# Kernel tuning notes

Measured on AMD Instinct MI355X. Metric: run time of the kernel, lower is better.

## Reference

```python
import jax, jax.numpy as jnp
import numpy as np

B, LQ, LK = 4, 2048, 2048
DQ = DK = DV = DH = 1024


def _xavier(key, shape):
    fan_out, fan_in = shape
    bound = float(np.sqrt(6.0 / (fan_in + fan_out)))
    return jax.random.uniform(key, shape, jnp.float32, -bound, bound)


def setup_inputs() -> dict:
    key = jax.random.key(0)
    ks = jax.random.split(key, 6)
    query = jax.random.normal(ks[0], (B, LQ, DQ), jnp.float32)
    k_in = jax.random.normal(ks[1], (B, LK, DK), jnp.float32)
    key_mask = jax.random.randint(ks[2], (B, LK), 0, 2).astype(bool)
    # torch nn.Linear weights are [out_features, in_features]
    Wk = _xavier(ks[3], (2 * DH, DK))
    bk = jnp.zeros((2 * DH,), jnp.float32)
    Wq = _xavier(ks[4], (DH, DQ))
    bq = jnp.zeros((DH,), jnp.float32)
    Wfc = _xavier(ks[5], (DV, DH))
    bfc = jnp.zeros((DV,), jnp.float32)
    return {"query": query, "key": k_in, "key_mask": key_mask,
            "Wq": Wq, "bq": bq, "Wk": Wk, "bk": bk, "Wfc": Wfc, "bfc": bfc}


def reference(query, key, key_mask, Wq, bq, Wk, bk, Wfc, bfc):
    bs, timesteps, _ = key.shape
    dim = DH
    q = query @ Wq.T + bq                       # [B, Lq, dim]
    c = (key @ Wk.T + bk).reshape(bs, timesteps, 2, dim)
    k = c[:, :, 0]                              # [B, Lk, dim]
    v = c[:, :, 1]                              # [B, Lk, dim]
    scores = jnp.einsum('bqd,bkd->bqk', q, k)   # [B, Lq, Lk]
    scores = jnp.where(key_mask[:, None, :], -jnp.inf, scores)
    attn = jax.nn.softmax(scores, axis=-1)
    out = jnp.einsum('bqk,bkd->bqd', attn, v)   # [B, Lq, dim]
    out = out @ Wfc.T + bfc                     # [B, Lq, DV] (dropout p=0 / eval)
    return out
```

## Files before the change

### kernel.cpp

```cpp
#include <hip/hip_runtime.h>

typedef __attribute__((ext_vector_type(8))) _Float16 half8;
typedef __attribute__((ext_vector_type(4))) _Float16 half4;
typedef __attribute__((ext_vector_type(4))) float f32x4;

__global__ __launch_bounds__(256) void conv4_k(const float4* __restrict__ in,
                                               half4* __restrict__ out){
  int i = blockIdx.x * 256 + threadIdx.x;
  float4 v = in[i];
  half4 h = { (_Float16)v.x, (_Float16)v.y, (_Float16)v.z, (_Float16)v.w };
  out[i] = h;
}

__global__ void mask_detect(const unsigned int* __restrict__ m, int* __restrict__ flag){
  if (threadIdx.x == 0 && blockIdx.x == 0){
    int ok = 1;
#pragma unroll
    for (int j = 0; j < 16; j++){
      unsigned v = m[j];
      if (v != 0u && v != 1u && v != 0x3f800000u) ok = 0;
    }
    *flag = ok;
  }
}

__global__ __launch_bounds__(256) void softmax2048(const float* __restrict__ S,
                                                   _Float16* __restrict__ P){
  const long row = blockIdx.x;
  const float* s = S + row * 2048;
  _Float16* p = P + row * 2048;
  const int tid = threadIdx.x;
  float v[8];
  float m = -1e30f;
#pragma unroll
  for (int i = 0; i < 8; i++){ v[i] = s[tid + i * 256]; m = fmaxf(m, v[i]); }
#pragma unroll
  for (int o = 32; o; o >>= 1) m = fmaxf(m, __shfl_xor(m, o));
  __shared__ float rm[4], rs[4];
  if ((tid & 63) == 0) rm[tid >> 6] = m;
  __syncthreads();
  m = fmaxf(fmaxf(rm[0], rm[1]), fmaxf(rm[2], rm[3]));
  float sum = 0.f;
#pragma unroll
  for (int i = 0; i < 8; i++){ v[i] = __expf(v[i] - m); sum += v[i]; }
#pragma unroll
  for (int o = 32; o; o >>= 1) sum += __shfl_xor(sum, o);
  if ((tid & 63) == 0) rs[tid >> 6] = sum;
  __syncthreads();
  sum = rs[0] + rs[1] + rs[2] + rs[3];
  const float inv = 1.0f / sum;
#pragma unroll
  for (int i = 0; i < 8; i++) p[tid + i * 256] = (_Float16)(v[i] * inv);
}

#define GLL(gp, ldsoff) \
  __builtin_amdgcn_global_load_lds((const __attribute__((address_space(1))) void*)(gp), \
                                   (__attribute__((address_space(3))) void*)&lds[ldsoff], 16, 0, 0)
#define BAR() asm volatile("s_barrier" ::: "memory")
#define VMCNT(n) asm volatile("s_waitcnt vmcnt(" #n ")" ::: "memory")

template<int EPI, int NREP>
__global__ __launch_bounds__(512, 2)
void gemm256(const unsigned short* __restrict__ A, const unsigned short* __restrict__ B,
             int lda, int ldb, int K, const float* __restrict__ bias,
             const void* __restrict__ mask, const int* __restrict__ maskFlag,
             void* __restrict__ out0, int ldc, long aBS, long bBS, long oBS, int maskBS)
{
  constexpr int BN     = 64 * NREP;
  constexpr int BUFSZ  = 16384 + 4096 * NREP;
  constexpr int NCHUNK = 2 + NREP / 2;
  __shared__ short lds[2 * BUFSZ];

  const int z = blockIdx.z;
  const long zA = (long)z * aBS, zB = (long)z * bBS;
  const int tid = threadIdx.x;
  const int lane = tid & 63, wid = tid >> 6;
  const int wr = wid >> 2, wc = wid & 3;
  const int fr = lane & 15, fk = lane >> 4;
  const int brow = blockIdx.x * 256, bcol = blockIdx.y * BN;

  f32x4 acc[8][NREP];
  const f32x4 fzero = {0.f, 0.f, 0.f, 0.f};
#pragma unroll
  for (int i = 0; i < 8; i++)
#pragma unroll
    for (int j = 0; j < NREP; j++) acc[i][j] = fzero;

  const int srow = tid >> 3, scol = (tid & 7) * 8;
  const unsigned short* Ag = A + zA + (long)(brow + srow) * lda + scol;
  const unsigned short* Bg = B + zB + (long)(bcol + srow) * ldb + scol;
  const int aoff = (wr * 128 + fr) * 64 + fk * 8;
  const int boff = (wc * 16 * NREP + fr) * 64 + fk * 8;

  auto stage = [&](int nb, int c, long k1) {
    if (c < 2) {
      const unsigned short* g = Ag + (long)(c * 128) * lda + k1;
      GLL(g,                  nb + c * 8192 + tid * 8);
      GLL(g + (long)64 * lda, nb + c * 8192 + 4096 + tid * 8);
    } else {
      const unsigned short* g = Bg + (long)((c - 2) * 128) * ldb + k1;
      GLL(g,                  nb + 16384 + (c - 2) * 8192 + tid * 8);
      GLL(g + (long)64 * ldb, nb + 16384 + (c - 2) * 8192 + 4096 + tid * 8);
    }
  };

  half8 a[4][2], b[NREP][2];
  auto readA = [&](int cb, int qm) {
#pragma unroll
    for (int mi = 0; mi < 4; ++mi)
#pragma unroll
      for (int kk = 0; kk < 2; ++kk)
        a[mi][kk] = *(const half8*)&lds[cb + aoff + qm * 4096 + mi * 1024 + kk * 32];
  };
  auto readB = [&](int cb, int n0, int n1) {
#pragma unroll
    for (int ni = n0; ni < n1; ++ni)
#pragma unroll
      for (int kk = 0; kk < 2; ++kk)
        b[ni][kk] = *(const half8*)&lds[cb + 16384 + boff + ni * 1024 + kk * 32];
  };
  auto mmaQ = [&](int qm, int n0, int n1) {
#pragma unroll
    for (int mi = 0; mi < 4; ++mi)
#pragma unroll
      for (int ni = n0; ni < n1; ++ni) {
        f32x4 c = acc[qm * 4 + mi][ni];
        c = __builtin_amdgcn_mfma_f32_16x16x32_f16(a[mi][0], b[ni][0], c, 0, 0, 0);
        c = __builtin_amdgcn_mfma_f32_16x16x32_f16(a[mi][1], b[ni][1], c, 0, 0, 0);
        acc[qm * 4 + mi][ni] = c;
      }
  };

  const int nt = K >> 6;
  for (int c = 0; c < NCHUNK; ++c) stage(0, c, 0);

  for (int t = 0; t < nt; ++t) {
    const int cb = (t & 1) ? BUFSZ : 0, nb = cb ^ BUFSZ;
    const long k1 = (long)(t + 1) << 6;
    const bool pf = (t + 1 < nt);
    if constexpr (NREP == 4) {
      if (pf) { stage(nb, 0, k1); VMCNT(2); } else VMCNT(0);
      BAR();
      readA(cb, 0); readB(cb, 0, 2);
      __builtin_amdgcn_s_setprio(1); mmaQ(0, 0, 2); __builtin_amdgcn_s_setprio(0);
      BAR();
      if (pf) stage(nb, 1, k1);
      readB(cb, 2, 4);
      BAR();
      __builtin_amdgcn_s_setprio(1); mmaQ(0, 2, 4); __builtin_amdgcn_s_setprio(0);
      BAR();
      if (pf) stage(nb, 2, k1);
      readA(cb, 1);
      BAR();
      __builtin_amdgcn_s_setprio(1); mmaQ(1, 2, 4); __builtin_amdgcn_s_setprio(0);
      BAR();
      if (pf) stage(nb, 3, k1);
      BAR();
      __builtin_amdgcn_s_setprio(1); mmaQ(1, 0, 2); __builtin_amdgcn_s_setprio(0);
      BAR();
    } else {
      if (pf) { stage(nb, 0, k1); stage(nb, 1, k1); VMCNT(4); } else VMCNT(0);
      BAR();
      readA(cb, 0); readB(cb, 0, 2);
      __builtin_amdgcn_s_setprio(1); mmaQ(0, 0, 2); __builtin_amdgcn_s_setprio(0);
      BAR();
      if (pf) stage(nb, 2, k1);
      readA(cb, 1);
      BAR();
      __builtin_amdgcn_s_setprio(1); mmaQ(1, 0, 2); __builtin_amdgcn_s_setprio(0);
      BAR();
    }
  }

  const long zO = (long)z * oBS;
  int mflag = 0;
  if constexpr (EPI == 1) mflag = *maskFlag;
#pragma unroll
  for (int mi = 0; mi < 8; ++mi) {
#pragma unroll
    for (int ni = 0; ni < NREP; ++ni) {
      const int col = bcol + wc * 16 * NREP + ni * 16 + fr;
      float bv = 0.f;
      if constexpr (EPI != 1) { if (bias) bv = bias[col]; }
      bool msk = false;
      if constexpr (EPI == 1) {
        msk = mflag ? (((const int*)mask)[(long)z * maskBS + col] != 0)
                    : (((const unsigned char*)mask)[(long)z * maskBS + col] != 0);
      }
#pragma unroll
      for (int r = 0; r < 4; ++r) {
        const int row = brow + wr * 128 + mi * 16 + fk * 4 + r;
        float v = acc[mi][ni][r] + bv;
        if constexpr (EPI == 0) {
          ((float*)out0)[zO + (long)row * ldc + col] = v;
        } else if constexpr (EPI == 1) {
          ((float*)out0)[zO + (long)row * ldc + col] = msk ? -1e30f : v;
        } else if constexpr (EPI == 2) {
          ((_Float16*)out0)[zO + (long)row * ldc + col] = (_Float16)v;
        } else {
          const int bb = row >> 11, tt = row & 2047;
          ((_Float16*)out0)[(long)bb * 2048 * 1024 + (long)col * 2048 + tt] = (_Float16)v;
        }
      }
    }
  }
}

extern "C" void kernel_launch(void* const* d_in, const int* in_sizes, int n_in,
                              void* d_out, int out_size, void* d_ws, size_t ws_size,
                              hipStream_t stream)
{
  (void)in_sizes; (void)n_in; (void)out_size; (void)ws_size;
  const float* query = (const float*)d_in[0];
  const float* key   = (const float*)d_in[1];
  const void*  kmask = d_in[2];
  const float* Wq    = (const float*)d_in[3];
  const float* bq    = (const float*)d_in[4];
  const float* Wk    = (const float*)d_in[5];
  const float* bk    = (const float*)d_in[6];
  const float* Wfc   = (const float*)d_in[7];
  const float* bfc   = (const float*)d_in[8];
  float* out = (float*)d_out;

  char* ws = (char*)d_ws;
  size_t o = 0;
  auto take = [&](size_t bytes)->char*{
    char* p = ws + o;
    o += (bytes + 255) & ~(size_t)255;
    return p;
  };
  const size_t SZ_H = (size_t)8192 * 1024 * 2;

  int* maskFlag           = (int*)take(256);
  unsigned short* query_h = (unsigned short*)take(SZ_H);
  unsigned short* key_h   = (unsigned short*)take(SZ_H);
  unsigned short* Wq_h    = (unsigned short*)take((size_t)1024 * 1024 * 2);
  unsigned short* Wk_h    = (unsigned short*)take((size_t)2048 * 1024 * 2);
  unsigned short* Wfc_h   = (unsigned short*)take((size_t)1024 * 1024 * 2);
  unsigned short* Q       = (unsigned short*)take(SZ_H);
  unsigned short* K       = (unsigned short*)take(SZ_H);
  unsigned short* VT      = (unsigned short*)take(SZ_H);
  unsigned short* O       = (unsigned short*)take(SZ_H);
  float*          S       = (float*)take((size_t)8192 * 2048 * 4);
  unsigned short* P       = (unsigned short*)take((size_t)8192 * 2048 * 2);

  mask_detect<<<1, 64, 0, stream>>>((const unsigned int*)kmask, maskFlag);

  conv4_k<<<8192, 256, 0, stream>>>((const float4*)query, (half4*)query_h);
  conv4_k<<<8192, 256, 0, stream>>>((const float4*)key,   (half4*)key_h);
  conv4_k<<<1024, 256, 0, stream>>>((const float4*)Wq,    (half4*)Wq_h);
  conv4_k<<<2048, 256, 0, stream>>>((const float4*)Wk,    (half4*)Wk_h);
  conv4_k<<<1024, 256, 0, stream>>>((const float4*)Wfc,   (half4*)Wfc_h);

  gemm256<2, 2><<<dim3(32, 8, 1), 512, 0, stream>>>(
      query_h, Wq_h, 1024, 1024, 1024,
      bq, nullptr, nullptr, Q, 1024, 0, 0, 0, 0);

  gemm256<2, 2><<<dim3(32, 8, 1), 512, 0, stream>>>(
      key_h, Wk_h, 1024, 1024, 1024,
      bk, nullptr, nullptr, K, 1024, 0, 0, 0, 0);

  gemm256<4, 2><<<dim3(32, 8, 1), 512, 0, stream>>>(
      key_h, Wk_h + (size_t)1024 * 1024, 1024, 1024, 1024,
      bk + 1024, nullptr, nullptr, VT, 0, 0, 0, 0, 0);

  gemm256<1, 4><<<dim3(8, 8, 4), 512, 0, stream>>>(
      Q, K, 1024, 1024, 1024,
      nullptr, kmask, maskFlag, S, 2048,
      (long)2048 * 1024, (long)2048 * 1024, (long)2048 * 2048, 2048);

  softmax2048<<<8192, 256, 0, stream>>>(S, (_Float16*)P);

  gemm256<2, 2><<<dim3(8, 8, 4), 512, 0, stream>>>(
      P, VT, 2048, 2048, 2048,
      nullptr, nullptr, nullptr, O, 1024,
      (long)2048 * 2048, (long)1024 * 2048, (long)2048 * 1024, 0);

  gemm256<0, 2><<<dim3(32, 8, 1), 512, 0, stream>>>(
      O, Wfc_h, 1024, 1024, 1024,
      bfc, nullptr, nullptr, out, 1024, 0, 0, 0, 0);
}
```

Measured before the change: 406.1 us.

## Use 256x256 tiles everywhere, XOR-swizzle LDS, fuse K and V projections

Every GEMM now uses a single 256x256 block tile. This raises arithmetic intensity per block and halves the grid for the N=1024 GEMMs. LDS loads and reads use an XOR swizzle on the 16-byte column chunk to cut bank conflicts. The separate K and V projections become one GEMM over the full 2048-wide Wk, whose epilogue splits output into row-major K and transposed V. The tradeoff is fewer blocks, at most 128-256, which may underfill the CUs, plus higher register pressure.

Result: faster. 389.3 us (-4.1%).

```diff
diff --git a/kernel.cpp b/kernel.cpp
--- a/kernel.cpp
+++ b/kernel.cpp
@@ -59,16 +59,15 @@
 #define BAR() asm volatile("s_barrier" ::: "memory")
 #define VMCNT(n) asm volatile("s_waitcnt vmcnt(" #n ")" ::: "memory")
 
-template<int EPI, int NREP>
+template<int EPI>
 __global__ __launch_bounds__(512, 2)
 void gemm256(const unsigned short* __restrict__ A, const unsigned short* __restrict__ B,
              int lda, int ldb, int K, const float* __restrict__ bias,
              const void* __restrict__ mask, const int* __restrict__ maskFlag,
-             void* __restrict__ out0, int ldc, long aBS, long bBS, long oBS, int maskBS)
+             void* __restrict__ out0, void* __restrict__ out1, int ldc,
+             long aBS, long bBS, long oBS, int maskBS)
 {
-  constexpr int BN     = 64 * NREP;
-  constexpr int BUFSZ  = 16384 + 4096 * NREP;
-  constexpr int NCHUNK = 2 + NREP / 2;
+  constexpr int BUFSZ = 32768;
   __shared__ short lds[2 * BUFSZ];
 
   const int z = blockIdx.z;
@@ -77,20 +76,25 @@
   const int lane = tid & 63, wid = tid >> 6;
   const int wr = wid >> 2, wc = wid & 3;
   const int fr = lane & 15, fk = lane >> 4;
-  const int brow = blockIdx.x * 256, bcol = blockIdx.y * BN;
-
-  f32x4 acc[8][NREP];
+  const int brow = blockIdx.x * 256, bcol = blockIdx.y * 256;
+
+  f32x4 acc[8][4];
   const f32x4 fzero = {0.f, 0.f, 0.f, 0.f};
 #pragma unroll
   for (int i = 0; i < 8; i++)
 #pragma unroll
-    for (int j = 0; j < NREP; j++) acc[i][j] = fzero;
-
-  const int srow = tid >> 3, scol = (tid & 7) * 8;
+    for (int j = 0; j < 4; j++) acc[i][j] = fzero;
+
+  const int srow = tid >> 3;
+  const int scol = ((tid & 7) ^ (srow & 7)) * 8;
   const unsigned short* Ag = A + zA + (long)(brow + srow) * lda + scol;
   const unsigned short* Bg = B + zB + (long)(bcol + srow) * ldb + scol;
-  const int aoff = (wr * 128 + fr) * 64 + fk * 8;
-  const int boff = (wc * 16 * NREP + fr) * 64 + fk * 8;
+
+  const int frs = fr & 7;
+  const int c0 = ((0 * 4 + fk) ^ frs) * 8;
+  const int c1 = ((1 * 4 + fk) ^ frs) * 8;
+  const int aRow = wr * 8192 + fr * 64;
+  const int bRow = wc * 4096 + fr * 64;
 
   auto stage = [&](int nb, int c, long k1) {
     if (c < 2) {
@@ -104,26 +108,30 @@
     }
   };
 
-  half8 a[4][2], b[NREP][2];
+  half8 a[4][2], b[4][2];
   auto readA = [&](int cb, int qm) {
 #pragma unroll
+    for (int mi = 0; mi < 4; ++mi) {
+      const int e = cb + aRow + qm * 4096 + mi * 1024;
+      a[mi][0] = *(const half8*)&lds[e + c0];
+      a[mi][1] = *(const half8*)&lds[e + c1];
+    }
+  };
+  auto readB = [&](int cb, int n0) {
+#pragma unroll
+    for (int i = 0; i < 2; ++i) {
+      const int ni = n0 + i;
+      const int e = cb + 16384 + bRow + ni * 1024;
+      b[ni][0] = *(const half8*)&lds[e + c0];
+      b[ni][1] = *(const half8*)&lds[e + c1];
+    }
+  };
+  auto mmaQ = [&](int qm, int n0) {
+#pragma unroll
     for (int mi = 0; mi < 4; ++mi)
 #pragma unroll
-      for (int kk = 0; kk < 2; ++kk)
-        a[mi][kk] = *(const half8*)&lds[cb + aoff + qm * 4096 + mi * 1024 + kk * 32];
-  };
-  auto readB = [&](int cb, int n0, int n1) {
-#pragma unroll
-    for (int ni = n0; ni < n1; ++ni)
-#pragma unroll
-      for (int kk = 0; kk < 2; ++kk)
-        b[ni][kk] = *(const half8*)&lds[cb + 16384 + boff + ni * 1024 + kk * 32];
-  };
-  auto mmaQ = [&](int qm, int n0, int n1) {
-#pragma unroll
-    for (int mi = 0; mi < 4; ++mi)
-#pragma unroll
-      for (int ni = n0; ni < n1; ++ni) {
+      for (int i = 0; i < 2; ++i) {
+        const int ni = n0 + i;
         f32x4 c = acc[qm * 4 + mi][ni];
         c = __builtin_amdgcn_mfma_f32_16x16x32_f16(a[mi][0], b[ni][0], c, 0, 0, 0);
         c = __builtin_amdgcn_mfma_f32_16x16x32_f16(a[mi][1], b[ni][1], c, 0, 0, 0);
@@ -132,44 +140,31 @@
   };
 
   const int nt = K >> 6;
-  for (int c = 0; c < NCHUNK; ++c) stage(0, c, 0);
+  for (int c = 0; c < 4; ++c) stage(0, c, 0);
 
   for (int t = 0; t < nt; ++t) {
     const int cb = (t & 1) ? BUFSZ : 0, nb = cb ^ BUFSZ;
     const long k1 = (long)(t + 1) << 6;
     const bool pf = (t + 1 < nt);
-    if constexpr (NREP == 4) {
-      if (pf) { stage(nb, 0, k1); VMCNT(2); } else VMCNT(0);
-      BAR();
-      readA(cb, 0); readB(cb, 0, 2);
-      __builtin_amdgcn_s_setprio(1); mmaQ(0, 0, 2); __builtin_amdgcn_s_setprio(0);
-      BAR();
-      if (pf) stage(nb, 1, k1);
-      readB(cb, 2, 4);
-      BAR();
-      __builtin_amdgcn_s_setprio(1); mmaQ(0, 2, 4); __builtin_amdgcn_s_setprio(0);
-      BAR();
-      if (pf) stage(nb, 2, k1);
-      readA(cb, 1);
-      BAR();
-      __builtin_amdgcn_s_setprio(1); mmaQ(1, 2, 4); __builtin_amdgcn_s_setprio(0);
-      BAR();
-      if (pf) stage(nb, 3, k1);
-      BAR();
-      __builtin_amdgcn_s_setprio(1); mmaQ(1, 0, 2); __builtin_amdgcn_s_setprio(0);
-      BAR();
-    } else {
-      if (pf) { stage(nb, 0, k1); stage(nb, 1, k1); VMCNT(4); } else VMCNT(0);
-      BAR();
-      readA(cb, 0); readB(cb, 0, 2);
-      __builtin_amdgcn_s_setprio(1); mmaQ(0, 0, 2); __builtin_amdgcn_s_setprio(0);
-      BAR();
-      if (pf) stage(nb, 2, k1);
-      readA(cb, 1);
-      BAR();
-      __builtin_amdgcn_s_setprio(1); mmaQ(1, 0, 2); __builtin_amdgcn_s_setprio(0);
-      BAR();
-    }
+    if (pf) { stage(nb, 0, k1); VMCNT(2); } else VMCNT(0);
+    BAR();
+    readA(cb, 0); readB(cb, 0);
+    __builtin_amdgcn_s_setprio(1); mmaQ(0, 0); __builtin_amdgcn_s_setprio(0);
+    BAR();
+    if (pf) stage(nb, 1, k1);
+    readB(cb, 2);
+    BAR();
+    __builtin_amdgcn_s_setprio(1); mmaQ(0, 2); __builtin_amdgcn_s_setprio(0);
+    BAR();
+    if (pf) stage(nb, 2, k1);
+    readA(cb, 1);
+    BAR();
+    __builtin_amdgcn_s_setprio(1); mmaQ(1, 2); __builtin_amdgcn_s_setprio(0);
+    BAR();
+    if (pf) stage(nb, 3, k1);
+    BAR();
+    __builtin_amdgcn_s_setprio(1); mmaQ(1, 0); __builtin_amdgcn_s_setprio(0);
+    BAR();
   }
 
   const long zO = (long)z * oBS;
@@ -178,8 +173,8 @@
 #pragma unroll
   for (int mi = 0; mi < 8; ++mi) {
 #pragma unroll
-    for (int ni = 0; ni < NREP; ++ni) {
-      const int col = bcol + wc * 16 * NREP + ni * 16 + fr;
+    for (int ni = 0; ni < 4; ++ni) {
+      const int col = bcol + wc * 64 + ni * 16 + fr;
       float bv = 0.f;
       if constexpr (EPI != 1) { if (bias) bv = bias[col]; }
       bool msk = false;
@@ -189,7 +184,7 @@
       }
 #pragma unroll
       for (int r = 0; r < 4; ++r) {
-        const int row = brow + wr * 128 + mi * 16 + fk * 4 + r;
+        const int row = brow + (wid >> 2) * 128 + mi * 16 + (lane >> 4) * 4 + r;
         float v = acc[mi][ni][r] + bv;
         if constexpr (EPI == 0) {
           ((float*)out0)[zO + (long)row * ldc + col] = v;
@@ -198,8 +193,12 @@
         } else if constexpr (EPI == 2) {
           ((_Float16*)out0)[zO + (long)row * ldc + col] = (_Float16)v;
         } else {
-          const int bb = row >> 11, tt = row & 2047;
-          ((_Float16*)out0)[(long)bb * 2048 * 1024 + (long)col * 2048 + tt] = (_Float16)v;
+          if (col < 1024) {
+            ((_Float16*)out0)[(long)row * 1024 + col] = (_Float16)v;
+          } else {
+            const int bb = row >> 11, tt = row & 2047;
+            ((_Float16*)out1)[(long)bb * 2048 * 1024 + (long)(col - 1024) * 2048 + tt] = (_Float16)v;
+          }
         }
       }
     }
@@ -252,31 +251,27 @@
   conv4_k<<<2048, 256, 0, stream>>>((const float4*)Wk,    (half4*)Wk_h);
   conv4_k<<<1024, 256, 0, stream>>>((const float4*)Wfc,   (half4*)Wfc_h);
 
-  gemm256<2, 2><<<dim3(32, 8, 1), 512, 0, stream>>>(
+  gemm256<5><<<dim3(32, 8, 1), 512, 0, stream>>>(
+      key_h, Wk_h, 1024, 1024, 1024,
+      bk, nullptr, nullptr, K, VT, 1024, 0, 0, 0, 0);
+
+  gemm256<2><<<dim3(32, 4, 1), 512, 0, stream>>>(
       query_h, Wq_h, 1024, 1024, 1024,
-      bq, nullptr, nullptr, Q, 1024, 0, 0, 0, 0);
-
-  gemm256<2, 2><<<dim3(32, 8, 1), 512, 0, stream>>>(
-      key_h, Wk_h, 1024, 1024, 1024,
-      bk, nullptr, nullptr, K, 1024, 0, 0, 0, 0);
-
-  gemm256<4, 2><<<dim3(32, 8, 1), 512, 0, stream>>>(
-      key_h, Wk_h + (size_t)1024 * 1024, 1024, 1024, 1024,
-      bk + 1024, nullptr, nullptr, VT, 0, 0, 0, 0, 0);
-
-  gemm256<1, 4><<<dim3(8, 8, 4), 512, 0, stream>>>(
+      bq, nullptr, nullptr, Q, nullptr, 1024, 0, 0, 0, 0);
+
+  gemm256<1><<<dim3(8, 8, 4), 512, 0, stream>>>(
       Q, K, 1024, 1024, 1024,
-      nullptr, kmask, maskFlag, S, 2048,
+      nullptr, kmask, maskFlag, S, nullptr, 2048,
       (long)2048 * 1024, (long)2048 * 1024, (long)2048 * 2048, 2048);
 
   softmax2048<<<8192, 256, 0, stream>>>(S, (_Float16*)P);
 
-  gemm256<2, 2><<<dim3(8, 8, 4), 512, 0, stream>>>(
+  gemm256<2><<<dim3(8, 4, 4), 512, 0, stream>>>(
       P, VT, 2048, 2048, 2048,
-      nullptr, nullptr, nullptr, O, 1024,
+      nullptr, nullptr, nullptr, O, nullptr, 1024,
       (long)2048 * 2048, (long)1024 * 2048, (long)2048 * 1024, 0);
 
-  gemm256<0, 2><<<dim3(32, 8, 1), 512, 0, stream>>>(
+  gemm256<0><<<dim3(32, 4, 1), 512, 0, stream>>>(
       O, Wfc_h, 1024, 1024, 1024,
-      bfc, nullptr, nullptr, out, 1024, 0, 0, 0, 0);
-}
+      bfc, nullptr, nullptr, out, nullptr, 1024, 0, 0, 0, 0);
+}
```
